# Kernel tuning notes

Hardware: AMD Instinct MI355X
Metric: run time of the kernel (lower is better)

Reference implementation:

```python
import jax, jax.numpy as jnp
import numpy as np

# ---- static circuit configuration (from init_kwargs) ----
N_Q, N_L, N_A = 8, 3, 2
N_REC = N_L * N_A            # deferred-measurement record wires (measure+reset per layer/ancilla)
T = N_Q + N_A + N_REC        # 16 total wires -> 2^16 state vector
ANC = list(range(N_Q, N_Q + N_A))
C64 = jnp.complex64

# ---- constant gate matrices ----
H = (np.array([[1, 1], [1, -1]]) / np.sqrt(2)).astype(np.complex64)
SWAP = np.array([[1,0,0,0],[0,0,1,0],[0,1,0,0],[0,0,0,1]], np.complex64)
_X = np.array([[0,1],[1,0]]); _Y = np.array([[0,-1j],[1j,0]])
XX = np.kron(_X, _X).astype(np.complex64)
YY = np.kron(_Y, _Y).astype(np.complex64)
I4 = np.eye(4, dtype=np.complex64)
# doubly-controlled RX(pi/4): controls = (record wire, q1), target = q2
_th = np.pi / 4
CCRX = np.eye(8, dtype=np.complex64)
CCRX[6,6] = CCRX[7,7] = np.cos(_th/2)
CCRX[6,7] = CCRX[7,6] = -1j*np.sin(_th/2)

# ---- parameterized gate builders ----
def _rx(t):
    c = jnp.cos(t/2).astype(C64); s = (-1j*jnp.sin(t/2)).astype(C64)
    return jnp.stack([jnp.stack([c, s]), jnp.stack([s, c])])

def _ry(t):
    c = jnp.cos(t/2); s = jnp.sin(t/2)
    return jnp.stack([jnp.stack([c, -s]), jnp.stack([s, c])]).astype(C64)

def _rz(t):
    e = jnp.exp(-0.5j*t).astype(C64)
    return jnp.diag(jnp.stack([e, jnp.conj(e)]))

def _rxx(t):
    return (jnp.cos(t/2)*I4 - 1j*jnp.sin(t/2)*XX).astype(C64)

def _ryy(t):
    return (jnp.cos(t/2)*I4 - 1j*jnp.sin(t/2)*YY).astype(C64)

def _rzz(t):
    e = jnp.exp(-0.5j*t).astype(C64); f = jnp.conj(e)
    return jnp.diag(jnp.stack([e, f, f, e]))

def _crz(t):  # control first, target second
    e = jnp.exp(-0.5j*t).astype(C64); one = jnp.ones((), C64)
    return jnp.diag(jnp.stack([one, one, e, jnp.conj(e)]))

def _apply(state, U, wires):
    n = len(wires)
    U = jnp.asarray(U, C64).reshape((2,)*(2*n))
    state = jnp.tensordot(U, state, axes=(tuple(range(n, 2*n)), wires))
    return jnp.moveaxis(state, tuple(range(n)), wires)

def _simulate(x, weights, phase_weights):
    # single-sample state-vector simulation with deferred mid-circuit measurements
    state = jnp.zeros((2,)*T, C64).at[(0,)*T].set(1.0)
    for q in range(N_Q):
        state = _apply(state, H, (q,))
    rec = N_Q + N_A
    for layer in range(N_L):
        # AngleEmbedding: RY on even layers, RX on odd layers
        rot = _ry if layer % 2 == 0 else _rx
        for q in range(N_Q):
            state = _apply(state, rot(x[q]), (q,))
        # phase interference block
        pw = phase_weights[layer]
        for a in ANC:
            state = _apply(state, H, (a,))
        for i, a in enumerate(ANC):
            for j in range(N_Q):
                state = _apply(state, _crz(pw[i, j]), (j, a))
        # adaptive measurement (deferred): optional H, then swap ancilla to fresh record wire (= measure + reset)
        recs = []
        for a in ANC:
            if layer % 2 == 1:
                state = _apply(state, H, (a,))
            state = _apply(state, SWAP, (a, rec))
            recs.append(rec); rec += 1
        # parallel exchange network
        w = weights[layer]
        pairs = [(i, i+1) for i in range(0, N_Q-1, 2)]
        for i, (q1, q2) in enumerate(pairs):
            state = _apply(state, _rxx(w[3*i]), (q1, q2))
            state = _apply(state, _ryy(w[3*i+1]), (q1, q2))
            state = _apply(state, _rzz(w[3*i+2]), (q1, q2))
            if i < N_A:  # qml.cond(m_i, CRX)(pi/4) -> record-controlled CRX
                state = _apply(state, CCRX, (recs[i], q1, q2))
        off = [(i, i+1) for i in range(1, N_Q-1, 2)]
        for i, (q1, q2) in enumerate(off):
            idx = len(pairs) + i
            if 3*idx + 2 < w.shape[0]:
                state = _apply(state, _rxx(w[3*idx]), (q1, q2))
                state = _apply(state, _ryy(w[3*idx+1]), (q1, q2))
                state = _apply(state, _rzz(w[3*idx+2]), (q1, q2))
        # single-qubit variational layer on the last n_qubits*3 params
        vw = w[-N_Q*3:]
        for q in range(N_Q):
            state = _apply(state, _rx(vw[3*q]), (q,))
            state = _apply(state, _ry(vw[3*q+1]), (q,))
            state = _apply(state, _rz(vw[3*q+2]), (q,))
    # <Z_q> for the data qubits
    probs = jnp.abs(state)**2
    evs = []
    for q in range(N_Q):
        m = probs.sum(axis=tuple(a for a in range(T) if a != q))
        evs.append(m[0] - m[1])
    return jnp.stack(evs).astype(jnp.float32)


def setup_inputs() -> dict:
    key = jax.random.key(0)
    k1, k2, k3 = jax.random.split(key, 3)
    x = jax.random.normal(k1, (16, N_Q), jnp.float32)
    weights = jax.random.normal(k2, (N_L, max(N_Q*6, 24)), jnp.float32) * 0.1
    phase_weights = jax.random.normal(k3, (N_L, N_A, N_Q), jnp.float32) * 0.1
    return {"x": x, "weights": weights, "phase_weights": phase_weights}


def reference(x, weights, phase_weights):
    return jax.vmap(_simulate, in_axes=(0, None, None))(x, weights, phase_weights)
```

## Files before the change

### kernel.cpp

```cpp
#include <hip/hip_runtime.h>
#include <cstdint>


struct F2 { float x, y; };

__device__ __forceinline__ F2 cmul(F2 a, F2 b) {
  return F2{ a.x * b.x - a.y * b.y, a.x * b.y + a.y * b.x };
}
__device__ __forceinline__ F2 cfma2(F2 a, F2 b, F2 c) {
  return F2{ fmaf(a.x, b.x, fmaf(-a.y, b.y, c.x)),
             fmaf(a.x, b.y, fmaf( a.y, b.x, c.y)) };
}

template<uint32_t MASK>
__device__ __forceinline__ uint32_t pdep10(uint32_t x) {
  uint32_t r = 0;
  #pragma unroll
  for (int b = 0; b < 10; ++b) {
    if (MASK & (1u << b)) { r |= (x & 1u) << b; x >>= 1; }
  }
  return r;
}

__device__ __forceinline__ uint32_t sw(uint32_t i) { return i ^ ((i >> 5) & 31u); }

template<uint32_t MASK>
__device__ __forceinline__ void readGrp(const F2* lds, int lane, F2 a[16]) {
  const uint32_t base = pdep10<(~MASK) & 0x3FFu>((uint32_t)lane);
  #pragma unroll
  for (uint32_t j = 0; j < 16; ++j) a[j] = lds[sw(base | pdep10<MASK>(j))];
}
template<uint32_t MASK>
__device__ __forceinline__ void writeGrp(F2* lds, int lane, const F2 a[16]) {
  const uint32_t base = pdep10<(~MASK) & 0x3FFu>((uint32_t)lane);
  #pragma unroll
  for (uint32_t j = 0; j < 16; ++j) lds[sw(base | pdep10<MASK>(j))] = a[j];
}

__device__ __forceinline__ void gate1(F2 a[16], const F2 U[4], int p) {
  const int s = 1 << p;
  #pragma unroll
  for (int i = 0; i < 16; ++i) {
    if (i & s) continue;
    F2 a0 = a[i], a1 = a[i | s];
    a[i]     = cfma2(U[0], a0, cmul(U[1], a1));
    a[i | s] = cfma2(U[2], a0, cmul(U[3], a1));
  }
}

__device__ __forceinline__ void gateH(F2 a[16], int p) {
  const float R = 0.70710678118654752f;
  const int s = 1 << p;
  #pragma unroll
  for (int i = 0; i < 16; ++i) {
    if (i & s) continue;
    F2 a0 = a[i], a1 = a[i | s];
    a[i]     = F2{ (a0.x + a1.x) * R, (a0.y + a1.y) * R };
    a[i | s] = F2{ (a0.x - a1.x) * R, (a0.y - a1.y) * R };
  }
}

__device__ __forceinline__ void gateM4(F2 a[16], const F2 m[4], int p, int q) {
  const int sp = 1 << p, sq = 1 << q;
  #pragma unroll
  for (int i = 0; i < 16; ++i) {
    if (i & (sp | sq)) continue;
    F2 v0 = a[i], v1 = a[i | sq], v2 = a[i | sp], v3 = a[i | sp | sq];
    a[i]           = cfma2(m[0], v0, cmul(m[2], v3));
    a[i | sp | sq] = cfma2(m[2], v0, cmul(m[0], v3));
    a[i | sq]      = cfma2(m[1], v1, cmul(m[3], v2));
    a[i | sp]      = cfma2(m[3], v1, cmul(m[1], v2));
  }
}

__device__ __forceinline__ void gateCCRX(F2 a[16], int c1, int c2, int t) {
  const float C = 0.92387953251128674f;
  const float S = 0.38268343236508978f;
  const int cm = (1 << c1) | (1 << c2);
  const int st = 1 << t;
  #pragma unroll
  for (int i = 0; i < 16; ++i) {
    if ((i & (cm | st)) != cm) continue;
    F2 a0 = a[i], a1 = a[i | st];
    a[i]      = F2{ fmaf(C, a0.x,  S * a1.y), fmaf(C, a0.y, -S * a1.x) };
    a[i | st] = F2{ fmaf(C, a1.x,  S * a0.y), fmaf(C, a1.y, -S * a0.x) };
  }
}

__device__ __forceinline__ void rot_rx(F2 m[4], float t) {
  float c, s; __sincosf(0.5f * t, &s, &c);
  m[0] = F2{c, 0.f}; m[1] = F2{0.f, -s}; m[2] = F2{0.f, -s}; m[3] = F2{c, 0.f};
}
__device__ __forceinline__ void rot_ry(F2 m[4], float t) {
  float c, s; __sincosf(0.5f * t, &s, &c);
  m[0] = F2{c, 0.f}; m[1] = F2{-s, 0.f}; m[2] = F2{s, 0.f}; m[3] = F2{c, 0.f};
}
__device__ __forceinline__ void rot_rz(F2 m[4], float t) {
  float c, s; __sincosf(0.5f * t, &s, &c);
  m[0] = F2{c, -s}; m[1] = F2{0.f, 0.f}; m[2] = F2{0.f, 0.f}; m[3] = F2{c, s};
}
__device__ __forceinline__ void mat2mul(F2 o[4], const F2 A[4], const F2 B[4]) {
  o[0] = cfma2(A[0], B[0], cmul(A[1], B[2]));
  o[1] = cfma2(A[0], B[1], cmul(A[1], B[3]));
  o[2] = cfma2(A[2], B[0], cmul(A[3], B[2]));
  o[3] = cfma2(A[2], B[1], cmul(A[3], B[3]));
}

template<int L>
__global__ __launch_bounds__(64)
void qsim(const float* __restrict__ x, const float* __restrict__ w,
          const float* __restrict__ pwg, const F2* __restrict__ src,
          F2* __restrict__ dst, float* __restrict__ out)
{
  __shared__ F2 amp[1024];
  __shared__ F2 sUpre[8][4];
  __shared__ F2 sUpost[8][4];
  __shared__ F2 sM4[7][4];
  __shared__ float sPW[2][8];

  const int lane  = threadIdx.x;
  const int chunk = blockIdx.x;
  const int b = chunk >> (2 * L);
  const int s = chunk & ((1 << (2 * L)) - 1);

  if (L == 0 && blockIdx.x == 0) { out[lane] = 0.f; out[lane + 64] = 0.f; }

  if (lane < 8) {
    const int q = lane;
    F2 tail[4];
    if constexpr (L == 0) {
      const float R = 0.70710678118654752f;
      tail[0] = F2{R, 0.f}; tail[1] = F2{R, 0.f};
      tail[2] = F2{R, 0.f}; tail[3] = F2{-R, 0.f};
    } else {
      F2 rx[4], ry[4], rz[4], t0[4];
      rot_rx(rx, w[(L - 1) * 48 + 24 + 3 * q]);
      rot_ry(ry, w[(L - 1) * 48 + 24 + 3 * q + 1]);
      rot_rz(rz, w[(L - 1) * 48 + 24 + 3 * q + 2]);
      mat2mul(t0, ry, rx);
      mat2mul(tail, rz, t0);
    }
    F2 rot[4];
    if ((L & 1) == 0) rot_ry(rot, x[b * 8 + q]); else rot_rx(rot, x[b * 8 + q]);
    F2 u[4]; mat2mul(u, rot, tail);
    #pragma unroll
    for (int k = 0; k < 4; ++k) sUpre[q][k] = u[k];
  } else if (L == 2 && lane >= 8 && lane < 16) {
    const int q = lane - 8;
    F2 rx[4], ry[4], rz[4], t0[4], t1[4];
    rot_rx(rx, w[2 * 48 + 24 + 3 * q]);
    rot_ry(ry, w[2 * 48 + 24 + 3 * q + 1]);
    rot_rz(rz, w[2 * 48 + 24 + 3 * q + 2]);
    mat2mul(t0, ry, rx); mat2mul(t1, rz, t0);
    #pragma unroll
    for (int k = 0; k < 4; ++k) sUpost[q][k] = t1[k];
  } else if (lane >= 16 && lane < 23) {
    const int p = lane - 16;
    float cx, sx, cy, sy, cz, sz;
    __sincosf(0.5f * w[L * 48 + 3 * p    ], &sx, &cx);
    __sincosf(0.5f * w[L * 48 + 3 * p + 1], &sy, &cy);
    __sincosf(0.5f * w[L * 48 + 3 * p + 2], &sz, &cz);
    const F2 e  = F2{cz, -sz};
    const F2 eb = F2{cz,  sz};
    const float P = cx * cy + sx * sy, Q = cx * cy - sx * sy;
    sM4[p][0] = F2{ e.x * P,  e.y * P };
    sM4[p][1] = F2{ eb.x * Q, eb.y * Q };
    sM4[p][2] = cmul(e,  F2{0.f,  sy * cx - sx * cy});
    sM4[p][3] = cmul(eb, F2{0.f, -(sx * cy + sy * cx)});
  } else if (lane >= 24 && lane < 32) {
    const int j = lane - 24;
    sPW[0][j] = pwg[L * 16 + j];
    sPW[1][j] = pwg[L * 16 + 8 + j];
  }
  __syncthreads();

  F2 a[16];

  if constexpr (L == 0) {
    F2 lf = F2{1.f, 0.f};
    #pragma unroll
    for (int t = 0; t < 6; ++t) {
      const int bit = (lane >> t) & 1;
      F2 col = bit ? sUpre[2 + t][2] : sUpre[2 + t][0];
      lf = cmul(lf, col);
    }
    F2 c01[4];
    #pragma unroll
    for (int dd = 0; dd < 4; ++dd)
      c01[dd] = cmul((dd & 1) ? sUpre[0][2] : sUpre[0][0],
                     (dd & 2) ? sUpre[1][2] : sUpre[1][0]);
    #pragma unroll
    for (int j = 0; j < 16; ++j)
      a[j] = (j >> 2) ? F2{0.f, 0.f} : cmul(lf, c01[j & 3]);
  } else {
    const F2* sp = src + ((L == 1) ? (b * 1024 + s * 256) : (b * 4096 + s * 256));
    #pragma unroll
    for (int j = 0; j < 16; ++j) {
      const int d = j | ((lane & 15) << 4);
      a[j] = (lane >> 4) ? F2{0.f, 0.f} : sp[d];
    }
    gate1(a, sUpre[0], 0); gate1(a, sUpre[1], 1);
    gate1(a, sUpre[2], 2); gate1(a, sUpre[3], 3);
    writeGrp<0x00Fu>(amp, lane, a);
    __syncthreads();
    readGrp<0x0F0u>(amp, lane, a);
    gate1(a, sUpre[4], 0); gate1(a, sUpre[5], 1);
    gate1(a, sUpre[6], 2); gate1(a, sUpre[7], 3);
    writeGrp<0x0F0u>(amp, lane, a);
    __syncthreads();
    readGrp<0x303u>(amp, lane, a);
  }

  gateH(a, 2); gateH(a, 3);
  {
    float base0 = 0.f, base1 = 0.f;
    #pragma unroll
    for (int t = 0; t < 6; ++t) {
      const float bit = (float)((lane >> t) & 1);
      base0 += bit * sPW[0][2 + t];
      base1 += bit * sPW[1][2 + t];
    }
    const float pw00 = sPW[0][0], pw01 = sPW[0][1];
    const float pw10 = sPW[1][0], pw11 = sPW[1][1];
    #pragma unroll
    for (int dd = 0; dd < 4; ++dd) {
      const float w0 = 0.5f * (base0 + (dd & 1) * pw00 + ((dd >> 1) & 1) * pw01);
      const float w1 = 0.5f * (base1 + (dd & 1) * pw10 + ((dd >> 1) & 1) * pw11);
      float c0, s0, c1, s1;
      __sincosf(w0, &s0, &c0);
      __sincosf(w1, &s1, &c1);
      #pragma unroll
      for (int aa = 0; aa < 4; ++aa) {
        F2 f0 = F2{ c0, (aa & 1) ? s0 : -s0 };
        F2 f1 = F2{ c1, (aa & 2) ? s1 : -s1 };
        const int j = dd | (aa << 2);
        a[j] = cmul(a[j], cmul(f0, f1));
      }
    }
  }
  if (L == 1) { gateH(a, 2); gateH(a, 3); }
  gateM4(a, sM4[0], 0, 1);
  gateCCRX(a, 2, 0, 1);
  writeGrp<0x303u>(amp, lane, a);
  __syncthreads();

  readGrp<0x20Eu>(amp, lane, a);
  gateM4(a, sM4[1], 1, 2);
  gateCCRX(a, 3, 1, 2);
  gateM4(a, sM4[4], 0, 1);
  writeGrp<0x20Eu>(amp, lane, a);
  __syncthreads();

  readGrp<0x0F0u>(amp, lane, a);
  gateM4(a, sM4[2], 0, 1);
  gateM4(a, sM4[3], 2, 3);
  writeGrp<0x0F0u>(amp, lane, a);
  __syncthreads();

  readGrp<0x078u>(amp, lane, a);
  gateM4(a, sM4[5], 0, 1);
  gateM4(a, sM4[6], 2, 3);
  if constexpr (L == 2) {
    gate1(a, sUpost[3], 0); gate1(a, sUpost[4], 1);
    gate1(a, sUpost[5], 2); gate1(a, sUpost[6], 3);
  }
  writeGrp<0x078u>(amp, lane, a);
  __syncthreads();

  if constexpr (L < 2) {
    #pragma unroll
    for (int r = 0; r < 16; ++r) {
      const int i = r * 64 + lane;
      F2 v = amp[sw((uint32_t)i)];
      if (L == 0) dst[b * 1024 + i] = v;
      else        dst[b * 4096 + s * 256 + (i >> 8) * 1024 + (i & 255)] = v;
    }
  } else {
    readGrp<0x087u>(amp, lane, a);
    gate1(a, sUpost[0], 0); gate1(a, sUpost[1], 1);
    gate1(a, sUpost[2], 2); gate1(a, sUpost[7], 3);
    float T = 0.f, E0 = 0.f, E1 = 0.f, E2 = 0.f, E7 = 0.f;
    #pragma unroll
    for (int j = 0; j < 16; ++j) {
      const float p = a[j].x * a[j].x + a[j].y * a[j].y;
      T += p;
      E0 += (j & 1) ? -p : p;
      E1 += (j & 2) ? -p : p;
      E2 += (j & 4) ? -p : p;
      E7 += (j & 8) ? -p : p;
    }
    float ev[8];
    ev[0] = E0; ev[1] = E1; ev[2] = E2; ev[7] = E7;
    ev[3] = ((lane >> 0) & 1) ? -T : T;
    ev[4] = ((lane >> 1) & 1) ? -T : T;
    ev[5] = ((lane >> 2) & 1) ? -T : T;
    ev[6] = ((lane >> 3) & 1) ? -T : T;
    #pragma unroll
    for (int q = 0; q < 8; ++q) {
      float v = ev[q];
      #pragma unroll
      for (int k = 1; k < 64; k <<= 1) v += __shfl_xor(v, k, 64);
      if (lane == 0) atomicAdd(&out[b * 8 + q], v);
    }
  }
}

extern "C" void kernel_launch(void* const* d_in, const int* in_sizes, int n_in,
                              void* d_out, int out_size, void* d_ws, size_t ws_size,
                              hipStream_t stream) {
  (void)in_sizes; (void)n_in; (void)out_size; (void)ws_size;
  const float* x   = (const float*)d_in[0];
  const float* w   = (const float*)d_in[1];
  const float* pwg = (const float*)d_in[2];
  float* out = (float*)d_out;
  F2* wsA = (F2*)d_ws;
  F2* wsB = wsA + 16 * 1024;

  qsim<0><<<16,  64, 0, stream>>>(x, w, pwg, nullptr, wsA, out);
  qsim<1><<<64,  64, 0, stream>>>(x, w, pwg, wsA,     wsB, out);
  qsim<2><<<256, 64, 0, stream>>>(x, w, pwg, wsB,  nullptr, out);
}
```

Before: 85.88 us.

## Fuse three layer kernels into one with redundant per-block recomputation

Replaces the three per-layer launches, which pass state through global workspace, with one kernel of 256 blocks. Each block recomputes layer 0 and layer 1 for its batch element in shared memory and picks out its 256-amplitude slice between layers, so no global intermediate state is needed. A small zeroing kernel runs first. This removes launch overhead and global round-trips at the cost of redundant recomputation of the earlier layers in every block.

```diff
diff --git a/kernel.cpp b/kernel.cpp
--- a/kernel.cpp
+++ b/kernel.cpp
@@ -107,121 +107,21 @@
 }
 
 template<int L>
-__global__ __launch_bounds__(64)
-void qsim(const float* __restrict__ x, const float* __restrict__ w,
-          const float* __restrict__ pwg, const F2* __restrict__ src,
-          F2* __restrict__ dst, float* __restrict__ out)
+__device__ __forceinline__ void layer_tail(F2 a[16], F2* amp, int lane,
+    const F2 (*M4)[4], const float* PW0, const float* PW1,
+    const F2 (*Upost)[4])
 {
-  __shared__ F2 amp[1024];
-  __shared__ F2 sUpre[8][4];
-  __shared__ F2 sUpost[8][4];
-  __shared__ F2 sM4[7][4];
-  __shared__ float sPW[2][8];
-
-  const int lane  = threadIdx.x;
-  const int chunk = blockIdx.x;
-  const int b = chunk >> (2 * L);
-  const int s = chunk & ((1 << (2 * L)) - 1);
-
-  if (L == 0 && blockIdx.x == 0) { out[lane] = 0.f; out[lane + 64] = 0.f; }
-
-  if (lane < 8) {
-    const int q = lane;
-    F2 tail[4];
-    if constexpr (L == 0) {
-      const float R = 0.70710678118654752f;
-      tail[0] = F2{R, 0.f}; tail[1] = F2{R, 0.f};
-      tail[2] = F2{R, 0.f}; tail[3] = F2{-R, 0.f};
-    } else {
-      F2 rx[4], ry[4], rz[4], t0[4];
-      rot_rx(rx, w[(L - 1) * 48 + 24 + 3 * q]);
-      rot_ry(ry, w[(L - 1) * 48 + 24 + 3 * q + 1]);
-      rot_rz(rz, w[(L - 1) * 48 + 24 + 3 * q + 2]);
-      mat2mul(t0, ry, rx);
-      mat2mul(tail, rz, t0);
-    }
-    F2 rot[4];
-    if ((L & 1) == 0) rot_ry(rot, x[b * 8 + q]); else rot_rx(rot, x[b * 8 + q]);
-    F2 u[4]; mat2mul(u, rot, tail);
-    #pragma unroll
-    for (int k = 0; k < 4; ++k) sUpre[q][k] = u[k];
-  } else if (L == 2 && lane >= 8 && lane < 16) {
-    const int q = lane - 8;
-    F2 rx[4], ry[4], rz[4], t0[4], t1[4];
-    rot_rx(rx, w[2 * 48 + 24 + 3 * q]);
-    rot_ry(ry, w[2 * 48 + 24 + 3 * q + 1]);
-    rot_rz(rz, w[2 * 48 + 24 + 3 * q + 2]);
-    mat2mul(t0, ry, rx); mat2mul(t1, rz, t0);
-    #pragma unroll
-    for (int k = 0; k < 4; ++k) sUpost[q][k] = t1[k];
-  } else if (lane >= 16 && lane < 23) {
-    const int p = lane - 16;
-    float cx, sx, cy, sy, cz, sz;
-    __sincosf(0.5f * w[L * 48 + 3 * p    ], &sx, &cx);
-    __sincosf(0.5f * w[L * 48 + 3 * p + 1], &sy, &cy);
-    __sincosf(0.5f * w[L * 48 + 3 * p + 2], &sz, &cz);
-    const F2 e  = F2{cz, -sz};
-    const F2 eb = F2{cz,  sz};
-    const float P = cx * cy + sx * sy, Q = cx * cy - sx * sy;
-    sM4[p][0] = F2{ e.x * P,  e.y * P };
-    sM4[p][1] = F2{ eb.x * Q, eb.y * Q };
-    sM4[p][2] = cmul(e,  F2{0.f,  sy * cx - sx * cy});
-    sM4[p][3] = cmul(eb, F2{0.f, -(sx * cy + sy * cx)});
-  } else if (lane >= 24 && lane < 32) {
-    const int j = lane - 24;
-    sPW[0][j] = pwg[L * 16 + j];
-    sPW[1][j] = pwg[L * 16 + 8 + j];
-  }
-  __syncthreads();
-
-  F2 a[16];
-
-  if constexpr (L == 0) {
-    F2 lf = F2{1.f, 0.f};
-    #pragma unroll
-    for (int t = 0; t < 6; ++t) {
-      const int bit = (lane >> t) & 1;
-      F2 col = bit ? sUpre[2 + t][2] : sUpre[2 + t][0];
-      lf = cmul(lf, col);
-    }
-    F2 c01[4];
-    #pragma unroll
-    for (int dd = 0; dd < 4; ++dd)
-      c01[dd] = cmul((dd & 1) ? sUpre[0][2] : sUpre[0][0],
-                     (dd & 2) ? sUpre[1][2] : sUpre[1][0]);
-    #pragma unroll
-    for (int j = 0; j < 16; ++j)
-      a[j] = (j >> 2) ? F2{0.f, 0.f} : cmul(lf, c01[j & 3]);
-  } else {
-    const F2* sp = src + ((L == 1) ? (b * 1024 + s * 256) : (b * 4096 + s * 256));
-    #pragma unroll
-    for (int j = 0; j < 16; ++j) {
-      const int d = j | ((lane & 15) << 4);
-      a[j] = (lane >> 4) ? F2{0.f, 0.f} : sp[d];
-    }
-    gate1(a, sUpre[0], 0); gate1(a, sUpre[1], 1);
-    gate1(a, sUpre[2], 2); gate1(a, sUpre[3], 3);
-    writeGrp<0x00Fu>(amp, lane, a);
-    __syncthreads();
-    readGrp<0x0F0u>(amp, lane, a);
-    gate1(a, sUpre[4], 0); gate1(a, sUpre[5], 1);
-    gate1(a, sUpre[6], 2); gate1(a, sUpre[7], 3);
-    writeGrp<0x0F0u>(amp, lane, a);
-    __syncthreads();
-    readGrp<0x303u>(amp, lane, a);
-  }
-
   gateH(a, 2); gateH(a, 3);
   {
     float base0 = 0.f, base1 = 0.f;
     #pragma unroll
     for (int t = 0; t < 6; ++t) {
       const float bit = (float)((lane >> t) & 1);
-      base0 += bit * sPW[0][2 + t];
-      base1 += bit * sPW[1][2 + t];
+      base0 += bit * PW0[2 + t];
+      base1 += bit * PW1[2 + t];
     }
-    const float pw00 = sPW[0][0], pw01 = sPW[0][1];
-    const float pw10 = sPW[1][0], pw11 = sPW[1][1];
+    const float pw00 = PW0[0], pw01 = PW0[1];
+    const float pw10 = PW1[0], pw11 = PW1[1];
     #pragma unroll
     for (int dd = 0; dd < 4; ++dd) {
       const float w0 = 0.5f * (base0 + (dd & 1) * pw00 + ((dd >> 1) & 1) * pw01);
@@ -239,84 +139,199 @@
     }
   }
   if (L == 1) { gateH(a, 2); gateH(a, 3); }
-  gateM4(a, sM4[0], 0, 1);
+  gateM4(a, M4[0], 0, 1);
   gateCCRX(a, 2, 0, 1);
   writeGrp<0x303u>(amp, lane, a);
   __syncthreads();
 
   readGrp<0x20Eu>(amp, lane, a);
-  gateM4(a, sM4[1], 1, 2);
+  gateM4(a, M4[1], 1, 2);
   gateCCRX(a, 3, 1, 2);
-  gateM4(a, sM4[4], 0, 1);
+  gateM4(a, M4[4], 0, 1);
   writeGrp<0x20Eu>(amp, lane, a);
   __syncthreads();
 
   readGrp<0x0F0u>(amp, lane, a);
-  gateM4(a, sM4[2], 0, 1);
-  gateM4(a, sM4[3], 2, 3);
+  gateM4(a, M4[2], 0, 1);
+  gateM4(a, M4[3], 2, 3);
   writeGrp<0x0F0u>(amp, lane, a);
   __syncthreads();
 
   readGrp<0x078u>(amp, lane, a);
-  gateM4(a, sM4[5], 0, 1);
-  gateM4(a, sM4[6], 2, 3);
+  gateM4(a, M4[5], 0, 1);
+  gateM4(a, M4[6], 2, 3);
   if constexpr (L == 2) {
-    gate1(a, sUpost[3], 0); gate1(a, sUpost[4], 1);
-    gate1(a, sUpost[5], 2); gate1(a, sUpost[6], 3);
+    gate1(a, Upost[3], 0); gate1(a, Upost[4], 1);
+    gate1(a, Upost[5], 2); gate1(a, Upost[6], 3);
   }
   writeGrp<0x078u>(amp, lane, a);
   __syncthreads();
-
-  if constexpr (L < 2) {
-    #pragma unroll
-    for (int r = 0; r < 16; ++r) {
-      const int i = r * 64 + lane;
-      F2 v = amp[sw((uint32_t)i)];
-      if (L == 0) dst[b * 1024 + i] = v;
-      else        dst[b * 4096 + s * 256 + (i >> 8) * 1024 + (i & 255)] = v;
+}
+
+__device__ __forceinline__ void layer_head(F2 a[16], F2* amp, int lane,
+                                           const F2 (*Upre)[4])
+{
+  gate1(a, Upre[0], 0); gate1(a, Upre[1], 1);
+  gate1(a, Upre[2], 2); gate1(a, Upre[3], 3);
+  writeGrp<0x00Fu>(amp, lane, a);
+  __syncthreads();
+  readGrp<0x0F0u>(amp, lane, a);
+  gate1(a, Upre[4], 0); gate1(a, Upre[5], 1);
+  gate1(a, Upre[6], 2); gate1(a, Upre[7], 3);
+  writeGrp<0x0F0u>(amp, lane, a);
+  __syncthreads();
+  readGrp<0x303u>(amp, lane, a);
+}
+
+__device__ __forceinline__ void extract_slice(const F2* amp, int lane, int sel,
+                                              F2 a[16])
+{
+  #pragma unroll
+  for (int j = 0; j < 16; ++j) {
+    const int d = j | ((lane & 15) << 4);
+    F2 v = amp[sw((uint32_t)(d | (sel << 8)))];
+    a[j] = (lane >> 4) ? F2{0.f, 0.f} : v;
+  }
+  __syncthreads();
+}
+
+__global__ __launch_bounds__(128) void zero_out_k(float* out) {
+  out[threadIdx.x] = 0.f;
+}
+
+__global__ __launch_bounds__(64)
+void qpie_fused(const float* __restrict__ x, const float* __restrict__ w,
+                const float* __restrict__ pwg, float* __restrict__ out)
+{
+  __shared__ F2 amp[1024];
+  __shared__ F2 sUpre[3][8][4];
+  __shared__ F2 sUpost[8][4];
+  __shared__ F2 sM4[3][7][4];
+  __shared__ float sPW[3][2][8];
+
+  const int lane = threadIdx.x;
+  const int blk  = blockIdx.x;
+  const int b  = blk >> 4;
+  const int s1 = (blk >> 2) & 3;
+  const int s2 = blk & 3;
+
+  if (lane < 24) {
+    const int Lp = lane >> 3, q = lane & 7;
+    F2 tail[4];
+    if (Lp == 0) {
+      const float R = 0.70710678118654752f;
+      tail[0] = F2{R, 0.f}; tail[1] = F2{R, 0.f};
+      tail[2] = F2{R, 0.f}; tail[3] = F2{-R, 0.f};
+    } else {
+      F2 rx[4], ry[4], rz[4], t0[4];
+      rot_rx(rx, w[(Lp - 1) * 48 + 24 + 3 * q]);
+      rot_ry(ry, w[(Lp - 1) * 48 + 24 + 3 * q + 1]);
+      rot_rz(rz, w[(Lp - 1) * 48 + 24 + 3 * q + 2]);
+      mat2mul(t0, ry, rx);
+      mat2mul(tail, rz, t0);
     }
-  } else {
-    readGrp<0x087u>(amp, lane, a);
-    gate1(a, sUpost[0], 0); gate1(a, sUpost[1], 1);
-    gate1(a, sUpost[2], 2); gate1(a, sUpost[7], 3);
-    float T = 0.f, E0 = 0.f, E1 = 0.f, E2 = 0.f, E7 = 0.f;
-    #pragma unroll
-    for (int j = 0; j < 16; ++j) {
-      const float p = a[j].x * a[j].x + a[j].y * a[j].y;
-      T += p;
-      E0 += (j & 1) ? -p : p;
-      E1 += (j & 2) ? -p : p;
-      E2 += (j & 4) ? -p : p;
-      E7 += (j & 8) ? -p : p;
+    F2 rot[4];
+    if ((Lp & 1) == 0) rot_ry(rot, x[b * 8 + q]); else rot_rx(rot, x[b * 8 + q]);
+    F2 u[4]; mat2mul(u, rot, tail);
+    #pragma unroll
+    for (int k = 0; k < 4; ++k) sUpre[Lp][q][k] = u[k];
+  } else if (lane < 45) {
+    const int t = lane - 24;
+    const int Lp = t / 7, p = t % 7;
+    float cx, sx, cy, sy, cz, sz;
+    __sincosf(0.5f * w[Lp * 48 + 3 * p    ], &sx, &cx);
+    __sincosf(0.5f * w[Lp * 48 + 3 * p + 1], &sy, &cy);
+    __sincosf(0.5f * w[Lp * 48 + 3 * p + 2], &sz, &cz);
+    const F2 e  = F2{cz, -sz};
+    const F2 eb = F2{cz,  sz};
+    const float P = cx * cy + sx * sy, Q = cx * cy - sx * sy;
+    sM4[Lp][p][0] = F2{ e.x * P,  e.y * P };
+    sM4[Lp][p][1] = F2{ eb.x * Q, eb.y * Q };
+    sM4[Lp][p][2] = cmul(e,  F2{0.f,  sy * cx - sx * cy});
+    sM4[Lp][p][3] = cmul(eb, F2{0.f, -(sx * cy + sy * cx)});
+  } else if (lane < 53) {
+    const int q = lane - 45;
+    F2 rx[4], ry[4], rz[4], t0[4], t1[4];
+    rot_rx(rx, w[2 * 48 + 24 + 3 * q]);
+    rot_ry(ry, w[2 * 48 + 24 + 3 * q + 1]);
+    rot_rz(rz, w[2 * 48 + 24 + 3 * q + 2]);
+    mat2mul(t0, ry, rx); mat2mul(t1, rz, t0);
+    #pragma unroll
+    for (int k = 0; k < 4; ++k) sUpost[q][k] = t1[k];
+  } else if (lane >= 56) {
+    const int k = lane - 56;
+    float* pf = &sPW[0][0][0];
+    #pragma unroll
+    for (int m = 0; m < 6; ++m) pf[k * 6 + m] = pwg[k * 6 + m];
+  }
+  __syncthreads();
+
+  F2 a[16];
+
+  {
+    F2 lf = F2{1.f, 0.f};
+    #pragma unroll
+    for (int t = 0; t < 6; ++t) {
+      const int bit = (lane >> t) & 1;
+      F2 col = bit ? sUpre[0][2 + t][2] : sUpre[0][2 + t][0];
+      lf = cmul(lf, col);
     }
-    float ev[8];
-    ev[0] = E0; ev[1] = E1; ev[2] = E2; ev[7] = E7;
-    ev[3] = ((lane >> 0) & 1) ? -T : T;
-    ev[4] = ((lane >> 1) & 1) ? -T : T;
-    ev[5] = ((lane >> 2) & 1) ? -T : T;
-    ev[6] = ((lane >> 3) & 1) ? -T : T;
-    #pragma unroll
-    for (int q = 0; q < 8; ++q) {
-      float v = ev[q];
-      #pragma unroll
-      for (int k = 1; k < 64; k <<= 1) v += __shfl_xor(v, k, 64);
-      if (lane == 0) atomicAdd(&out[b * 8 + q], v);
-    }
+    F2 c01[4];
+    #pragma unroll
+    for (int dd = 0; dd < 4; ++dd)
+      c01[dd] = cmul((dd & 1) ? sUpre[0][0][2] : sUpre[0][0][0],
+                     (dd & 2) ? sUpre[0][1][2] : sUpre[0][1][0]);
+    #pragma unroll
+    for (int j = 0; j < 16; ++j)
+      a[j] = (j >> 2) ? F2{0.f, 0.f} : cmul(lf, c01[j & 3]);
+  }
+  layer_tail<0>(a, amp, lane, sM4[0], sPW[0][0], sPW[0][1], sUpost);
+
+  extract_slice(amp, lane, s1, a);
+  layer_head(a, amp, lane, sUpre[1]);
+  layer_tail<1>(a, amp, lane, sM4[1], sPW[1][0], sPW[1][1], sUpost);
+
+  extract_slice(amp, lane, s2, a);
+  layer_head(a, amp, lane, sUpre[2]);
+  layer_tail<2>(a, amp, lane, sM4[2], sPW[2][0], sPW[2][1], sUpost);
+
+  readGrp<0x087u>(amp, lane, a);
+  gate1(a, sUpost[0], 0); gate1(a, sUpost[1], 1);
+  gate1(a, sUpost[2], 2); gate1(a, sUpost[7], 3);
+  float T = 0.f, E0 = 0.f, E1 = 0.f, E2 = 0.f, E7 = 0.f;
+  #pragma unroll
+  for (int j = 0; j < 16; ++j) {
+    const float p = a[j].x * a[j].x + a[j].y * a[j].y;
+    T += p;
+    E0 += (j & 1) ? -p : p;
+    E1 += (j & 2) ? -p : p;
+    E2 += (j & 4) ? -p : p;
+    E7 += (j & 8) ? -p : p;
+  }
+  float ev[8];
+  ev[0] = E0; ev[1] = E1; ev[2] = E2; ev[7] = E7;
+  ev[3] = ((lane >> 0) & 1) ? -T : T;
+  ev[4] = ((lane >> 1) & 1) ? -T : T;
+  ev[5] = ((lane >> 2) & 1) ? -T : T;
+  ev[6] = ((lane >> 3) & 1) ? -T : T;
+  #pragma unroll
+  for (int q = 0; q < 8; ++q) {
+    float v = ev[q];
+    #pragma unroll
+    for (int k = 1; k < 64; k <<= 1) v += __shfl_xor(v, k, 64);
+    if (lane == 0) atomicAdd(&out[b * 8 + q], v);
   }
 }
 
 extern "C" void kernel_launch(void* const* d_in, const int* in_sizes, int n_in,
                               void* d_out, int out_size, void* d_ws, size_t ws_size,
                               hipStream_t stream) {
-  (void)in_sizes; (void)n_in; (void)out_size; (void)ws_size;
+  (void)in_sizes; (void)n_in; (void)out_size; (void)d_ws; (void)ws_size;
   const float* x   = (const float*)d_in[0];
   const float* w   = (const float*)d_in[1];
   const float* pwg = (const float*)d_in[2];
   float* out = (float*)d_out;
-  F2* wsA = (F2*)d_ws;
-  F2* wsB = wsA + 16 * 1024;
-
-  qsim<0><<<16,  64, 0, stream>>>(x, w, pwg, nullptr, wsA, out);
-  qsim<1><<<64,  64, 0, stream>>>(x, w, pwg, wsA,     wsB, out);
-  qsim<2><<<256, 64, 0, stream>>>(x, w, pwg, wsB,  nullptr, out);
-}
+
+  zero_out_k<<<1, 128, 0, stream>>>(out);
+  qpie_fused<<<256, 64, 0, stream>>>(x, w, pwg, out);
+}
```

After: 81.81 us. 4.7% less time.
